# Performance work log

Measured on AMD Instinct MI355X. Metric: run time of the kernel, lower is better.

The kernel has to match this reference:

```python
import jax, jax.numpy as jnp
import numpy as np

B, T, U, E, DIN = 32, 512, 1024, 1024, 256

def setup_inputs() -> dict:
    key = jax.random.key(0)
    ks = jax.random.split(key, 12)
    s = lambda d: 1.0 / np.sqrt(d)
    bias = jnp.zeros((4 * U,), jnp.float32).at[U:2 * U].set(2.0)  # forget-gate bias init = 2
    return {
        'inputs': jax.random.normal(ks[0], (B, DIN), jnp.float32),
        'h': jax.random.normal(ks[1], (B, U), jnp.float32) * 0.1,
        'c': jax.random.normal(ks[2], (B, U), jnp.float32) * 0.1,
        'speech_encode': jax.random.normal(ks[3], (B, T, E), jnp.float32),
        'encodestate': jax.random.normal(ks[4], (B, T, U), jnp.float32),
        'Wa_w': jax.random.normal(ks[5], (U, U), jnp.float32) * s(U),
        'Wa_b': jnp.zeros((U,), jnp.float32),
        'va_w': jax.random.normal(ks[6], (U, 1), jnp.float32) * s(U),
        'va_b': jnp.zeros((1,), jnp.float32),
        'kernel': jax.random.normal(ks[7], (DIN + E, 4 * U), jnp.float32) * s(DIN + E),
        'rec_kernel': jax.random.normal(ks[8], (U, 4 * U), jnp.float32) * s(U),
        'bias': bias,
    }


def reference(inputs, h, c, speech_encode, encodestate, Wa_w, Wa_b, va_w, va_b, kernel, rec_kernel, bias):
    # Bahdanau attention: score = va(tanh(Wa(h)[:,None,:] + encodestate))
    query = h @ Wa_w + Wa_b                                   # [B,U]
    scores = jnp.tanh(query[:, None, :] + encodestate) @ va_w  # [B,T,1]
    logits = jnp.squeeze(scores + va_b, axis=2)                # [B,T]
    attn = jax.nn.softmax(logits, axis=-1)                     # [B,T]
    context = jnp.einsum('bt,bte->be', attn, speech_encode)    # [B,E]
    # LSTM cell step on [inputs; context]
    x = jnp.concatenate([inputs, context], axis=1)             # [B,DIN+E]
    z = x @ kernel + h @ rec_kernel + bias                     # [B,4U]
    zi, zf, zg, zo = jnp.split(z, 4, axis=1)
    c_new = jax.nn.sigmoid(zf) * c + jax.nn.sigmoid(zi) * jnp.tanh(zg)
    h_new = jax.nn.sigmoid(zo) * jnp.tanh(c_new)
    return (h_new, h_new, c_new)  # (lstmout, [h, c])
```

## Files before the change

kernel.cpp:

```cpp
#include <hip/hip_runtime.h>
#include <hip/hip_bf16.h>

#define B 32
#define T 512
#define U 1024
#define E 1024
#define DIN 256
#define N4 4096

__device__ __forceinline__ float fast_tanh(float x) {
    float e = __expf(2.0f * x);
    return 1.0f - 2.0f / (e + 1.0f);
}
__device__ __forceinline__ float fast_sigmoid(float x) {
    return 1.0f / (1.0f + __expf(-x));
}

__global__ __launch_bounds__(256) void k1_query(const float* __restrict__ h,
                                                const float* __restrict__ Wa_w,
                                                float* __restrict__ qpart) {
    const int jc = blockIdx.x;
    const int kc = blockIdx.y;
    const int tid = threadIdx.x;
    const int k0 = kc * 32;
    __shared__ float hs[32][36];
    #pragma unroll
    for (int i = 0; i < 4; ++i) {
        int flat = i * 256 + tid;
        int kk = flat & 31, b = flat >> 5;
        hs[kk][b] = h[(size_t)b * U + k0 + kk];
    }
    __syncthreads();
    const int jg = tid & 31;
    const int bg = tid >> 5;
    const int ROWS = U / 4;
    const float4* Wp = (const float4*)(Wa_w + (size_t)k0 * U + jc * 128) + jg;
    float4 a0{}, a1{}, a2{}, a3{};
    float4 w0 = Wp[0 * ROWS], w1 = Wp[1 * ROWS], w2 = Wp[2 * ROWS], w3 = Wp[3 * ROWS];
#define K1_FMA(W, R)                                                            \
    {                                                                           \
        float4 x4 = *(const float4*)&hs[(R)][bg * 4];                           \
        a0.x += x4.x * (W).x; a0.y += x4.x * (W).y; a0.z += x4.x * (W).z; a0.w += x4.x * (W).w; \
        a1.x += x4.y * (W).x; a1.y += x4.y * (W).y; a1.z += x4.y * (W).z; a1.w += x4.y * (W).w; \
        a2.x += x4.z * (W).x; a2.y += x4.z * (W).y; a2.z += x4.z * (W).z; a2.w += x4.z * (W).w; \
        a3.x += x4.w * (W).x; a3.y += x4.w * (W).y; a3.z += x4.w * (W).z; a3.w += x4.w * (W).w; \
    }
    #pragma unroll 1
    for (int r = 0; r <= 24; r += 4) {
        float4 n0 = Wp[(r + 4) * ROWS], n1 = Wp[(r + 5) * ROWS];
        float4 n2 = Wp[(r + 6) * ROWS], n3 = Wp[(r + 7) * ROWS];
        K1_FMA(w0, r + 0); K1_FMA(w1, r + 1); K1_FMA(w2, r + 2); K1_FMA(w3, r + 3);
        w0 = n0; w1 = n1; w2 = n2; w3 = n3;
        if (r == 24) break;
    }
    K1_FMA(w0, 28); K1_FMA(w1, 29); K1_FMA(w2, 30); K1_FMA(w3, 31);
#undef K1_FMA
    float* q = qpart + ((size_t)(kc * 32 + bg * 4)) * U + jc * 128 + jg * 4;
    *(float4*)(q + 0 * U) = a0;
    *(float4*)(q + 1 * U) = a1;
    *(float4*)(q + 2 * U) = a2;
    *(float4*)(q + 3 * U) = a3;
}

__global__ __launch_bounds__(256) void k1b_qreduce(const float* __restrict__ qpart,
                                                   const float* __restrict__ Wa_b,
                                                   float* __restrict__ query) {
    int i = blockIdx.x * 256 + threadIdx.x;
    const float* p = qpart + i;
    float s = Wa_b[i & 1023];
    #pragma unroll
    for (int g = 0; g < 8; ++g) {
        float b0 = p[(size_t)(4 * g + 0) * 32768];
        float b1 = p[(size_t)(4 * g + 1) * 32768];
        float b2 = p[(size_t)(4 * g + 2) * 32768];
        float b3 = p[(size_t)(4 * g + 3) * 32768];
        s += b0 + b1 + b2 + b3;
    }
    query[i] = s;
}

__global__ __launch_bounds__(256) void k2_logits(const float* __restrict__ query,
                                                 const float* __restrict__ enc,
                                                 const float* __restrict__ va_w,
                                                 const float* __restrict__ va_b,
                                                 float* __restrict__ logits) {
    int gw = blockIdx.x * 4 + (threadIdx.x >> 6);
    int lane = threadIdx.x & 63;
    int b = gw >> 9, t = gw & 511;
    const float4* e4 = (const float4*)(enc + ((size_t)(b * T + t)) * U);
    const float4* q4 = (const float4*)(query + (size_t)b * U);
    const float4* v4 = (const float4*)va_w;
    float4 e[4], q[4], v[4];
    #pragma unroll
    for (int i = 0; i < 4; ++i) {
        int idx = i * 64 + lane;
        e[i] = e4[idx]; q[i] = q4[idx]; v[i] = v4[idx];
    }
    float acc = 0.f;
    #pragma unroll
    for (int i = 0; i < 4; ++i) {
        acc += fast_tanh(e[i].x + q[i].x) * v[i].x;
        acc += fast_tanh(e[i].y + q[i].y) * v[i].y;
        acc += fast_tanh(e[i].z + q[i].z) * v[i].z;
        acc += fast_tanh(e[i].w + q[i].w) * v[i].w;
    }
    #pragma unroll
    for (int off = 32; off > 0; off >>= 1) acc += __shfl_xor(acc, off);
    if (lane == 0) logits[b * T + t] = acc + va_b[0];
}

__global__ __launch_bounds__(256) void k3_softmax(const float* __restrict__ logits,
                                                  float* __restrict__ attn) {
    int b = blockIdx.x, tid = threadIdx.x, lane = tid & 63, w = tid >> 6;
    float l0 = logits[b * T + tid], l1 = logits[b * T + 256 + tid];
    float m = fmaxf(l0, l1);
    #pragma unroll
    for (int off = 32; off > 0; off >>= 1) m = fmaxf(m, __shfl_xor(m, off));
    __shared__ float sm[4], ss[4];
    if (lane == 0) sm[w] = m;
    __syncthreads();
    float M = fmaxf(fmaxf(sm[0], sm[1]), fmaxf(sm[2], sm[3]));
    float e0 = __expf(l0 - M), e1 = __expf(l1 - M);
    float s = e0 + e1;
    #pragma unroll
    for (int off = 32; off > 0; off >>= 1) s += __shfl_xor(s, off);
    if (lane == 0) ss[w] = s;
    __syncthreads();
    float inv = 1.0f / (ss[0] + ss[1] + ss[2] + ss[3]);
    attn[b * T + tid] = e0 * inv;
    attn[b * T + 256 + tid] = e1 * inv;
}

__global__ __launch_bounds__(256) void k4_ctx(const float* __restrict__ attn,
                                              const float* __restrict__ speech,
                                              float* __restrict__ ctxpart) {
    int bid = blockIdx.x;
    int eh = bid & 1, tc = (bid >> 1) & 15, b = bid >> 5;
    int t0 = tc * 32;
    __shared__ float sat[32];
    if (threadIdx.x < 32) sat[threadIdx.x] = attn[b * T + t0 + threadIdx.x];
    __syncthreads();
    int eg = threadIdx.x & 127;
    int ts = threadIdx.x >> 7;
    int e = eh * 512 + eg * 4;
    const int S = E / 4;
    const float4* sp = (const float4*)(speech + ((size_t)(b * T + t0 + ts * 16)) * E + e);
    float4 acc{};
    float4 p0 = sp[0 * S], p1 = sp[1 * S], p2 = sp[2 * S], p3 = sp[3 * S];
    const float* a = &sat[ts * 16];
    #pragma unroll 1
    for (int tt = 0; tt <= 8; tt += 4) {
        float4 n0 = sp[(size_t)(tt + 4) * S], n1 = sp[(size_t)(tt + 5) * S];
        float4 n2 = sp[(size_t)(tt + 6) * S], n3 = sp[(size_t)(tt + 7) * S];
        float c0 = a[tt + 0], c1 = a[tt + 1], c2 = a[tt + 2], c3 = a[tt + 3];
        acc.x += c0 * p0.x; acc.y += c0 * p0.y; acc.z += c0 * p0.z; acc.w += c0 * p0.w;
        acc.x += c1 * p1.x; acc.y += c1 * p1.y; acc.z += c1 * p1.z; acc.w += c1 * p1.w;
        acc.x += c2 * p2.x; acc.y += c2 * p2.y; acc.z += c2 * p2.z; acc.w += c2 * p2.w;
        acc.x += c3 * p3.x; acc.y += c3 * p3.y; acc.z += c3 * p3.z; acc.w += c3 * p3.w;
        p0 = n0; p1 = n1; p2 = n2; p3 = n3;
        if (tt == 8) break;
    }
    {
        float c0 = a[12], c1 = a[13], c2 = a[14], c3 = a[15];
        acc.x += c0 * p0.x; acc.y += c0 * p0.y; acc.z += c0 * p0.z; acc.w += c0 * p0.w;
        acc.x += c1 * p1.x; acc.y += c1 * p1.y; acc.z += c1 * p1.z; acc.w += c1 * p1.w;
        acc.x += c2 * p2.x; acc.y += c2 * p2.y; acc.z += c2 * p2.z; acc.w += c2 * p2.w;
        acc.x += c3 * p3.x; acc.y += c3 * p3.y; acc.z += c3 * p3.z; acc.w += c3 * p3.w;
    }
    int slice = tc * 2 + ts;
    *(float4*)(ctxpart + ((size_t)(slice * 32 + b)) * E + e) = acc;
}

__global__ __launch_bounds__(256) void k4b_ctxreduce(const float* __restrict__ ctxpart,
                                                     float* __restrict__ context) {
    int i = blockIdx.x * 256 + threadIdx.x;
    const float* p = ctxpart + i;
    float s = 0.f;
    #pragma unroll
    for (int g = 0; g < 8; ++g) {
        float b0 = p[(size_t)(4 * g + 0) * 32768];
        float b1 = p[(size_t)(4 * g + 1) * 32768];
        float b2 = p[(size_t)(4 * g + 2) * 32768];
        float b3 = p[(size_t)(4 * g + 3) * 32768];
        s += b0 + b1 + b2 + b3;
    }
    context[i] = s;
}

__device__ __forceinline__ void k5_stage(const char* gbase, int t, float* ldsbuf,
                                         int w, int lane) {
    #pragma unroll
    for (int i = 0; i < 4; ++i) {
        int flat = (w * 4 + i) * 1024 + lane * 16;
        int row = flat >> 9;
        int colb = flat & 511;
        const char* g = gbase + ((size_t)(t * 32 + row)) * (N4 * 4) + colb;
        char* l = (char*)ldsbuf + (size_t)(w * 4 + i) * 1024;
        __builtin_amdgcn_global_load_lds((const __attribute__((address_space(1))) void*)g,
                                         (__attribute__((address_space(3))) void*)l,
                                         16, 0, 0);
    }
}

__global__ __launch_bounds__(256) void k5_z(const float* __restrict__ xin,
                                            const float* __restrict__ ctx,
                                            const float* __restrict__ h,
                                            const float* __restrict__ Wk,
                                            const float* __restrict__ Wr,
                                            float* __restrict__ zpart) {
    const int jc = blockIdx.x;
    const int kc = blockIdx.y;
    const int tid = threadIdx.x;
    const int k0 = kc * 128;
    __shared__ float wtile[2][4096];
    __shared__ float xs[128][36];
    const float* xsrc; int xoff, xld;
    if (k0 < DIN)          { xsrc = xin; xoff = k0;           xld = DIN; }
    else if (k0 < DIN + E) { xsrc = ctx; xoff = k0 - DIN;     xld = E;   }
    else                   { xsrc = h;   xoff = k0 - DIN - E; xld = U;   }
    #pragma unroll
    for (int i = 0; i < 16; ++i) {
        int flat = i * 256 + tid;
        int kk = flat & 127, b = flat >> 7;
        xs[kk][b] = xsrc[(size_t)b * xld + xoff + kk];
    }
    const float* Wbase = (k0 < DIN + E) ? (Wk + (size_t)k0 * N4)
                                        : (Wr + (size_t)(k0 - DIN - E) * N4);
    const char* gtile = (const char*)(Wbase + jc * 128);
    const int w = tid >> 6, lane = tid & 63;
    const int jg = tid & 31, bg = tid >> 5;
    float4 a0{}, a1{}, a2{}, a3{};

    k5_stage(gtile, 0, wtile[0], w, lane);
    #pragma unroll
    for (int s = 0; s < 4; ++s) {
        if (s < 3) k5_stage(gtile, s + 1, wtile[(s + 1) & 1], w, lane);
        if (s == 0)      asm volatile("s_waitcnt vmcnt(4) lgkmcnt(0)" ::: "memory");
        else if (s < 3)  asm volatile("s_waitcnt vmcnt(4)" ::: "memory");
        else             asm volatile("s_waitcnt vmcnt(0)" ::: "memory");
        __builtin_amdgcn_s_barrier();
        const float* wb = wtile[s & 1];
        const int r0 = s * 32;
        #pragma unroll 8
        for (int r = 0; r < 32; ++r) {
            float4 w4 = *(const float4*)(wb + r * 128 + jg * 4);
            float4 x4 = *(const float4*)&xs[r0 + r][bg * 4];
            a0.x += x4.x * w4.x; a0.y += x4.x * w4.y; a0.z += x4.x * w4.z; a0.w += x4.x * w4.w;
            a1.x += x4.y * w4.x; a1.y += x4.y * w4.y; a1.z += x4.y * w4.z; a1.w += x4.y * w4.w;
            a2.x += x4.z * w4.x; a2.y += x4.z * w4.y; a2.z += x4.z * w4.z; a2.w += x4.z * w4.w;
            a3.x += x4.w * w4.x; a3.y += x4.w * w4.y; a3.z += x4.w * w4.z; a3.w += x4.w * w4.w;
        }
        __builtin_amdgcn_s_barrier();
    }
    float* zp = zpart + ((size_t)(kc * 32 + bg * 4)) * N4 + jc * 128 + jg * 4;
    *(float4*)(zp + 0 * N4) = a0;
    *(float4*)(zp + 1 * N4) = a1;
    *(float4*)(zp + 2 * N4) = a2;
    *(float4*)(zp + 3 * N4) = a3;
}

__global__ __launch_bounds__(256) void k6a_zreduce(const float* __restrict__ zpart,
                                                   const float* __restrict__ bias,
                                                   float* __restrict__ z) {
    int i = blockIdx.x * 256 + threadIdx.x;
    const float* p = zpart + i;
    float s = bias[i & 4095];
    #pragma unroll
    for (int g = 0; g < 4; ++g) {
        float b0 = p[(size_t)(4 * g + 0) * 131072];
        float b1 = p[(size_t)(4 * g + 1) * 131072];
        float b2 = p[(size_t)(4 * g + 2) * 131072];
        float b3 = p[(size_t)(4 * g + 3) * 131072];
        s += b0 + b1 + b2 + b3;
    }
    s += p[(size_t)16 * 131072] + p[(size_t)17 * 131072];
    z[i] = s;
}

__global__ __launch_bounds__(256) void k6b_gates(const float* __restrict__ z,
                                                 const float* __restrict__ c,
                                                 float* __restrict__ out) {
    int idx = blockIdx.x * 256 + threadIdx.x;
    int b = idx >> 10, u = idx & 1023;
    const float* zb = z + (size_t)b * N4;
    float zi = zb[u], zf = zb[U + u], zg = zb[2 * U + u], zo = zb[3 * U + u];
    float cn = fast_sigmoid(zf) * c[idx] + fast_sigmoid(zi) * fast_tanh(zg);
    float hn = fast_sigmoid(zo) * fast_tanh(cn);
    out[idx] = hn;
    out[32768 + idx] = hn;
    out[65536 + idx] = cn;
}

extern "C" void kernel_launch(void* const* d_in, const int* in_sizes, int n_in,
                              void* d_out, int out_size, void* d_ws, size_t ws_size,
                              hipStream_t stream) {
    const float* inputs = (const float*)d_in[0];
    const float* h      = (const float*)d_in[1];
    const float* c      = (const float*)d_in[2];
    const float* speech = (const float*)d_in[3];
    const float* enc    = (const float*)d_in[4];
    const float* Wa_w   = (const float*)d_in[5];
    const float* Wa_b   = (const float*)d_in[6];
    const float* va_w   = (const float*)d_in[7];
    const float* va_b   = (const float*)d_in[8];
    const float* Wk     = (const float*)d_in[9];
    const float* Wr     = (const float*)d_in[10];
    const float* bias   = (const float*)d_in[11];
    float* out = (float*)d_out;
    float* ws  = (float*)d_ws;

    float* big     = ws;
    float* qpart   = big;
    float* ctxpart = big;
    float* zpart   = big;
    float* z       = ws + 2359296;
    float* query   = ws + 2490368;
    float* context = ws + 2523136;
    float* logits  = ws + 2555904;
    float* attn    = ws + 2572288;

    k1_query<<<dim3(8, 32), 256, 0, stream>>>(h, Wa_w, qpart);
    k1b_qreduce<<<128, 256, 0, stream>>>(qpart, Wa_b, query);
    k2_logits<<<4096, 256, 0, stream>>>(query, enc, va_w, va_b, logits);
    k3_softmax<<<32, 256, 0, stream>>>(logits, attn);
    k4_ctx<<<1024, 256, 0, stream>>>(attn, speech, ctxpart);
    k4b_ctxreduce<<<128, 256, 0, stream>>>(ctxpart, context);
    k5_z<<<dim3(32, 18), 256, 0, stream>>>(inputs, context, h, Wk, Wr, zpart);
    k6a_zreduce<<<512, 256, 0, stream>>>(zpart, bias, z);
    k6b_gates<<<128, 256, 0, stream>>>(z, c, out);
}
```

Measured before the change: 226.0 us.

## Cut split-K for the LSTM gate GEMM and fuse the partial reduction into gates

The z GEMM now splits K into 8 chunks of 288 rows instead of 18 chunks of 128, launching 256 blocks instead of 576. Each chunk runs a 9-stage, 4-buffer async weight pipeline, and each wave now owns its own 32-column slice. The separate z-reduction kernel is removed: the gates kernel sums the 8 partials plus bias directly. This saves one launch and a write-then-read of the intermediate z buffer, and shrinks the partials traffic. In exchange it uses fewer blocks, with less latency hiding per CU, and more LDS per block.

Result: slower. 237.4 us (+5.0%).

```diff
diff --git a/kernel.cpp b/kernel.cpp
--- a/kernel.cpp
+++ b/kernel.cpp
@@ -7,6 +7,8 @@
 #define E 1024
 #define DIN 256
 #define N4 4096
+#define KCH 288
+#define NST 9
 
 __device__ __forceinline__ float fast_tanh(float x) {
     float e = __expf(2.0f * x);
@@ -187,15 +189,19 @@
     context[i] = s;
 }
 
-__device__ __forceinline__ void k5_stage(const char* gbase, int t, float* ldsbuf,
+__device__ __forceinline__ void k5_stage(const float* Wk, const float* Wr,
+                                         int k0, int t, int jc, float* buf,
                                          int w, int lane) {
     #pragma unroll
     for (int i = 0; i < 4; ++i) {
         int flat = (w * 4 + i) * 1024 + lane * 16;
         int row = flat >> 9;
         int colb = flat & 511;
-        const char* g = gbase + ((size_t)(t * 32 + row)) * (N4 * 4) + colb;
-        char* l = (char*)ldsbuf + (size_t)(w * 4 + i) * 1024;
+        int k = k0 + t * 32 + row;
+        const char* g = ((k < DIN + E) ? (const char*)(Wk + (size_t)k * N4)
+                                       : (const char*)(Wr + (size_t)(k - DIN - E) * N4))
+                        + jc * 512 + colb;
+        char* l = (char*)buf + (w * 4 + i) * 1024;
         __builtin_amdgcn_global_load_lds((const __attribute__((address_space(1))) void*)g,
                                          (__attribute__((address_space(3))) void*)l,
                                          16, 0, 0);
@@ -211,40 +217,44 @@
     const int jc = blockIdx.x;
     const int kc = blockIdx.y;
     const int tid = threadIdx.x;
-    const int k0 = kc * 128;
-    __shared__ float wtile[2][4096];
-    __shared__ float xs[128][36];
-    const float* xsrc; int xoff, xld;
-    if (k0 < DIN)          { xsrc = xin; xoff = k0;           xld = DIN; }
-    else if (k0 < DIN + E) { xsrc = ctx; xoff = k0 - DIN;     xld = E;   }
-    else                   { xsrc = h;   xoff = k0 - DIN - E; xld = U;   }
-    #pragma unroll
-    for (int i = 0; i < 16; ++i) {
-        int flat = i * 256 + tid;
-        int kk = flat & 127, b = flat >> 7;
-        xs[kk][b] = xsrc[(size_t)b * xld + xoff + kk];
-    }
-    const float* Wbase = (k0 < DIN + E) ? (Wk + (size_t)k0 * N4)
-                                        : (Wr + (size_t)(k0 - DIN - E) * N4);
-    const char* gtile = (const char*)(Wbase + jc * 128);
+    const int k0 = kc * KCH;
+    __shared__ float wt[4][4096];
+    __shared__ float xs[KCH][36];
+    #pragma unroll
+    for (int i = 0; i < 36; ++i) {
+        int f = i * 256 + tid;
+        int b = f / KCH, kk = f % KCH;
+        int k = k0 + kk;
+        float v;
+        if (k < DIN)          v = xin[b * DIN + k];
+        else if (k < DIN + E) v = ctx[b * E + (k - DIN)];
+        else                  v = h[b * U + (k - DIN - E)];
+        xs[kk][b] = v;
+    }
+    asm volatile("s_waitcnt vmcnt(0)" ::: "memory");
+
     const int w = tid >> 6, lane = tid & 63;
-    const int jg = tid & 31, bg = tid >> 5;
+    const int jg = lane & 7;
+    const int bg = lane >> 3;
     float4 a0{}, a1{}, a2{}, a3{};
 
-    k5_stage(gtile, 0, wtile[0], w, lane);
-    #pragma unroll
-    for (int s = 0; s < 4; ++s) {
-        if (s < 3) k5_stage(gtile, s + 1, wtile[(s + 1) & 1], w, lane);
-        if (s == 0)      asm volatile("s_waitcnt vmcnt(4) lgkmcnt(0)" ::: "memory");
-        else if (s < 3)  asm volatile("s_waitcnt vmcnt(4)" ::: "memory");
-        else             asm volatile("s_waitcnt vmcnt(0)" ::: "memory");
+    k5_stage(Wk, Wr, k0, 0, jc, wt[0], w, lane);
+    k5_stage(Wk, Wr, k0, 1, jc, wt[1], w, lane);
+    k5_stage(Wk, Wr, k0, 2, jc, wt[2], w, lane);
+    #pragma unroll
+    for (int s = 0; s < NST; ++s) {
+        if (s + 3 < NST) k5_stage(Wk, Wr, k0, s + 3, jc, wt[(s + 3) & 3], w, lane);
+        if (s == 0)           asm volatile("s_waitcnt vmcnt(12) lgkmcnt(0)" ::: "memory");
+        else if (s < NST - 3) asm volatile("s_waitcnt vmcnt(12)" ::: "memory");
+        else if (s == NST - 3) asm volatile("s_waitcnt vmcnt(8)" ::: "memory");
+        else if (s == NST - 2) asm volatile("s_waitcnt vmcnt(4)" ::: "memory");
+        else                  asm volatile("s_waitcnt vmcnt(0)" ::: "memory");
         __builtin_amdgcn_s_barrier();
-        const float* wb = wtile[s & 1];
-        const int r0 = s * 32;
+        const float* wb = wt[s & 3];
         #pragma unroll 8
         for (int r = 0; r < 32; ++r) {
-            float4 w4 = *(const float4*)(wb + r * 128 + jg * 4);
-            float4 x4 = *(const float4*)&xs[r0 + r][bg * 4];
+            float4 w4 = *(const float4*)(wb + r * 128 + w * 32 + jg * 4);
+            float4 x4 = *(const float4*)&xs[s * 32 + r][bg * 4];
             a0.x += x4.x * w4.x; a0.y += x4.x * w4.y; a0.z += x4.x * w4.z; a0.w += x4.x * w4.w;
             a1.x += x4.y * w4.x; a1.y += x4.y * w4.y; a1.z += x4.y * w4.z; a1.w += x4.y * w4.w;
             a2.x += x4.z * w4.x; a2.y += x4.z * w4.y; a2.z += x4.z * w4.z; a2.w += x4.z * w4.w;
@@ -252,38 +262,25 @@
         }
         __builtin_amdgcn_s_barrier();
     }
-    float* zp = zpart + ((size_t)(kc * 32 + bg * 4)) * N4 + jc * 128 + jg * 4;
+    float* zp = zpart + ((size_t)(kc * 32 + bg * 4)) * N4 + jc * 128 + w * 32 + jg * 4;
     *(float4*)(zp + 0 * N4) = a0;
     *(float4*)(zp + 1 * N4) = a1;
     *(float4*)(zp + 2 * N4) = a2;
     *(float4*)(zp + 3 * N4) = a3;
 }
 
-__global__ __launch_bounds__(256) void k6a_zreduce(const float* __restrict__ zpart,
-                                                   const float* __restrict__ bias,
-                                                   float* __restrict__ z) {
-    int i = blockIdx.x * 256 + threadIdx.x;
-    const float* p = zpart + i;
-    float s = bias[i & 4095];
-    #pragma unroll
-    for (int g = 0; g < 4; ++g) {
-        float b0 = p[(size_t)(4 * g + 0) * 131072];
-        float b1 = p[(size_t)(4 * g + 1) * 131072];
-        float b2 = p[(size_t)(4 * g + 2) * 131072];
-        float b3 = p[(size_t)(4 * g + 3) * 131072];
-        s += b0 + b1 + b2 + b3;
-    }
-    s += p[(size_t)16 * 131072] + p[(size_t)17 * 131072];
-    z[i] = s;
-}
-
-__global__ __launch_bounds__(256) void k6b_gates(const float* __restrict__ z,
-                                                 const float* __restrict__ c,
-                                                 float* __restrict__ out) {
+__global__ __launch_bounds__(256) void k6_gates(const float* __restrict__ zpart,
+                                                const float* __restrict__ bias,
+                                                const float* __restrict__ c,
+                                                float* __restrict__ out) {
     int idx = blockIdx.x * 256 + threadIdx.x;
     int b = idx >> 10, u = idx & 1023;
-    const float* zb = z + (size_t)b * N4;
-    float zi = zb[u], zf = zb[U + u], zg = zb[2 * U + u], zo = zb[3 * U + u];
+    float zi = bias[u], zf = bias[U + u], zg = bias[2 * U + u], zo = bias[3 * U + u];
+    #pragma unroll
+    for (int s = 0; s < 8; ++s) {
+        const float* zp = zpart + ((size_t)(s * 32 + b)) * N4;
+        zi += zp[u]; zf += zp[U + u]; zg += zp[2 * U + u]; zo += zp[3 * U + u];
+    }
     float cn = fast_sigmoid(zf) * c[idx] + fast_sigmoid(zi) * fast_tanh(zg);
     float hn = fast_sigmoid(zo) * fast_tanh(cn);
     out[idx] = hn;
@@ -313,11 +310,10 @@
     float* qpart   = big;
     float* ctxpart = big;
     float* zpart   = big;
-    float* z       = ws + 2359296;
-    float* query   = ws + 2490368;
-    float* context = ws + 2523136;
-    float* logits  = ws + 2555904;
-    float* attn    = ws + 2572288;
+    float* query   = ws + 1048576;
+    float* context = ws + 1081344;
+    float* logits  = ws + 1114112;
+    float* attn    = ws + 1130496;
 
     k1_query<<<dim3(8, 32), 256, 0, stream>>>(h, Wa_w, qpart);
     k1b_qreduce<<<128, 256, 0, stream>>>(qpart, Wa_b, query);
@@ -325,7 +321,6 @@
     k3_softmax<<<32, 256, 0, stream>>>(logits, attn);
     k4_ctx<<<1024, 256, 0, stream>>>(attn, speech, ctxpart);
     k4b_ctxreduce<<<128, 256, 0, stream>>>(ctxpart, context);
-    k5_z<<<dim3(32, 18), 256, 0, stream>>>(inputs, context, h, Wk, Wr, zpart);
-    k6a_zreduce<<<512, 256, 0, stream>>>(zpart, bias, z);
-    k6b_gates<<<128, 256, 0, stream>>>(z, c, out);
-}
+    k5_z<<<dim3(32, 8), 256, 0, stream>>>(inputs, context, h, Wk, Wr, zpart);
+    k6_gates<<<128, 256, 0, stream>>>(zpart, bias, c, out);
+}
```

## Fuse z split-K reduction into gate kernel and remap k5 thread tiling

Applied to the files above, without the earlier changes.

Removes the separate z reduction kernel and the intermediate z buffer. The gate kernel now sums the 18 split-K partials plus bias directly before applying the LSTM nonlinearities, which saves one launch and one global round trip. The k5 thread mapping also changes so that each wavefront covers a 32-column slice for all 32 batch rows, instead of 128 columns for 8 rows, which alters the LDS access pattern. The risk is that the fused kernel runs only 128 blocks doing 72 loads per thread, so it has less parallelism for the reduction than the old 512-block kernel.

Measured after the change: 224.7 us. No clear change (-0.6%).

```diff
diff --git a/kernel.cpp b/kernel.cpp
--- a/kernel.cpp
+++ b/kernel.cpp
@@ -228,7 +228,8 @@
                                         : (Wr + (size_t)(k0 - DIN - E) * N4);
     const char* gtile = (const char*)(Wbase + jc * 128);
     const int w = tid >> 6, lane = tid & 63;
-    const int jg = tid & 31, bg = tid >> 5;
+    const int jg = lane & 7;
+    const int bg = lane >> 3;
     float4 a0{}, a1{}, a2{}, a3{};
 
     k5_stage(gtile, 0, wtile[0], w, lane);
@@ -243,7 +244,7 @@
         const int r0 = s * 32;
         #pragma unroll 8
         for (int r = 0; r < 32; ++r) {
-            float4 w4 = *(const float4*)(wb + r * 128 + jg * 4);
+            float4 w4 = *(const float4*)(wb + r * 128 + w * 32 + jg * 4);
             float4 x4 = *(const float4*)&xs[r0 + r][bg * 4];
             a0.x += x4.x * w4.x; a0.y += x4.x * w4.y; a0.z += x4.x * w4.z; a0.w += x4.x * w4.w;
             a1.x += x4.y * w4.x; a1.y += x4.y * w4.y; a1.z += x4.y * w4.z; a1.w += x4.y * w4.w;
@@ -252,38 +253,25 @@
         }
         __builtin_amdgcn_s_barrier();
     }
-    float* zp = zpart + ((size_t)(kc * 32 + bg * 4)) * N4 + jc * 128 + jg * 4;
+    float* zp = zpart + ((size_t)(kc * 32 + bg * 4)) * N4 + jc * 128 + w * 32 + jg * 4;
     *(float4*)(zp + 0 * N4) = a0;
     *(float4*)(zp + 1 * N4) = a1;
     *(float4*)(zp + 2 * N4) = a2;
     *(float4*)(zp + 3 * N4) = a3;
 }
 
-__global__ __launch_bounds__(256) void k6a_zreduce(const float* __restrict__ zpart,
-                                                   const float* __restrict__ bias,
-                                                   float* __restrict__ z) {
-    int i = blockIdx.x * 256 + threadIdx.x;
-    const float* p = zpart + i;
-    float s = bias[i & 4095];
-    #pragma unroll
-    for (int g = 0; g < 4; ++g) {
-        float b0 = p[(size_t)(4 * g + 0) * 131072];
-        float b1 = p[(size_t)(4 * g + 1) * 131072];
-        float b2 = p[(size_t)(4 * g + 2) * 131072];
-        float b3 = p[(size_t)(4 * g + 3) * 131072];
-        s += b0 + b1 + b2 + b3;
-    }
-    s += p[(size_t)16 * 131072] + p[(size_t)17 * 131072];
-    z[i] = s;
-}
-
-__global__ __launch_bounds__(256) void k6b_gates(const float* __restrict__ z,
-                                                 const float* __restrict__ c,
-                                                 float* __restrict__ out) {
+__global__ __launch_bounds__(256) void k6_gates(const float* __restrict__ zpart,
+                                                const float* __restrict__ bias,
+                                                const float* __restrict__ c,
+                                                float* __restrict__ out) {
     int idx = blockIdx.x * 256 + threadIdx.x;
     int b = idx >> 10, u = idx & 1023;
-    const float* zb = z + (size_t)b * N4;
-    float zi = zb[u], zf = zb[U + u], zg = zb[2 * U + u], zo = zb[3 * U + u];
+    float zi = bias[u], zf = bias[U + u], zg = bias[2 * U + u], zo = bias[3 * U + u];
+    #pragma unroll
+    for (int s = 0; s < 18; ++s) {
+        const float* zp = zpart + ((size_t)(s * 32 + b)) * N4;
+        zi += zp[u]; zf += zp[U + u]; zg += zp[2 * U + u]; zo += zp[3 * U + u];
+    }
     float cn = fast_sigmoid(zf) * c[idx] + fast_sigmoid(zi) * fast_tanh(zg);
     float hn = fast_sigmoid(zo) * fast_tanh(cn);
     out[idx] = hn;
@@ -313,11 +301,10 @@
     float* qpart   = big;
     float* ctxpart = big;
     float* zpart   = big;
-    float* z       = ws + 2359296;
-    float* query   = ws + 2490368;
-    float* context = ws + 2523136;
-    float* logits  = ws + 2555904;
-    float* attn    = ws + 2572288;
+    float* query   = ws + 2359296;
+    float* context = ws + 2392064;
+    float* logits  = ws + 2424832;
+    float* attn    = ws + 2441216;
 
     k1_query<<<dim3(8, 32), 256, 0, stream>>>(h, Wa_w, qpart);
     k1b_qreduce<<<128, 256, 0, stream>>>(qpart, Wa_b, query);
@@ -326,6 +313,5 @@
     k4_ctx<<<1024, 256, 0, stream>>>(attn, speech, ctxpart);
     k4b_ctxreduce<<<128, 256, 0, stream>>>(ctxpart, context);
     k5_z<<<dim3(32, 18), 256, 0, stream>>>(inputs, context, h, Wk, Wr, zpart);
-    k6a_zreduce<<<512, 256, 0, stream>>>(zpart, bias, z);
-    k6b_gates<<<128, 256, 0, stream>>>(z, c, out);
-}
+    k6_gates<<<128, 256, 0, stream>>>(zpart, bias, c, out);
+}
```
